# Kernel optimization log

Measured on AMD Instinct MI355X. Metric: run time of the kernel, lower is better.

## Reference

```python
import jax, jax.numpy as jnp
import numpy as np

N = 8192        # num_nodes == total_gene_dim (required by A @ init_emb)
B = 4           # batch_size (number of graphs / perturbations)
E = 262144      # edges per graph (avg degree 32)
MAX_HOP = 4
EMBED = 64
HIDDEN = 512
OUT = 64
LN_EPS = 1e-5


def setup_inputs() -> dict:
    key = jax.random.key(0)
    ks = jax.random.split(key, 8)
    s = 0.02
    return {
        "edge_index": jax.random.randint(ks[0], (B, 2, E), 0, N, dtype=jnp.int32),
        "perturb_one_hot": jax.random.randint(ks[1], (B,), 0, N, dtype=jnp.int32),
        "proj_w": jax.random.normal(ks[2], (EMBED, B), dtype=jnp.float32) * s,
        "proj_b": jax.random.normal(ks[3], (EMBED,), dtype=jnp.float32) * s,
        "w1": jax.random.normal(ks[4], (HIDDEN, MAX_HOP * EMBED), dtype=jnp.float32) * s,
        "b1": jax.random.normal(ks[5], (HIDDEN,), dtype=jnp.float32) * s,
        "ln_g": jnp.ones((HIDDEN,), dtype=jnp.float32),
        "ln_b": jnp.zeros((HIDDEN,), dtype=jnp.float32),
        "w2": jax.random.normal(ks[6], (OUT, HIDDEN), dtype=jnp.float32) * s,
        "b2": jax.random.normal(ks[7], (OUT,), dtype=jnp.float32) * s,
    }


def reference(edge_index, perturb_one_hot, proj_w, proj_b, w1, b1, ln_g, ln_b, w2, b2):
    dt = proj_w.dtype
    # one_hot(perturb).T : (N, B) -> proj -> (N, EMBED)
    one_hot_mat = jax.nn.one_hot(perturb_one_hot, N, dtype=dt).T
    init_emb = one_hot_mat @ proj_w.T + proj_b  # (N, EMBED)

    def per_graph(ei):
        # coalesce() sums duplicate COO entries -> scatter-add of ones
        A = jnp.zeros((N, N), dtype=dt).at[ei[0], ei[1]].add(jnp.ones((E,), dtype=dt))
        H = A @ init_emb  # (N, EMBED); original recomputes the SAME product max_hop times
        omega = jnp.stack([H] * MAX_HOP, axis=-1).reshape(N, MAX_HOP * EMBED)
        h = omega @ w1.T + b1  # (N, HIDDEN)
        mu = h.mean(-1, keepdims=True)
        var = h.var(-1, keepdims=True)
        h = (h - mu) / jnp.sqrt(var + LN_EPS) * ln_g + ln_b
        h = jax.nn.gelu(h, approximate=False)  # torch GELU default is exact erf form
        return h @ w2.T + b2  # (N, OUT)

    return jax.vmap(per_graph)(edge_index)  # (B, N, OUT)
```

## Files before the change

kernel.cpp:

```cpp
#include <hip/hip_runtime.h>
#include <math.h>

#define NN   8192
#define NB   4
#define NE   262144
#define EMB  64
#define HID  512
#define NOUT 64
#define DMAX 256
#define SPEC_FLAG (1 << 30)
#define SLICES 32
#define HBLK (NB * SLICES)
#define HWORDS (NN / 2)

__device__ __forceinline__ void eval_block(
    float dg, float c0, float c1, float c2, float c3,
    const float* __restrict__ u, const float* __restrict__ b1,
    const float* __restrict__ ln_g, const float* __restrict__ ln_b,
    const float* __restrict__ w2t4, const float* __restrict__ b2,
    float* __restrict__ dst,
    float* __restrict__ g,
    float* __restrict__ pacc,
    float* __restrict__ red)
{
    int tid = threadIdx.x, lane = tid & 63, wid = tid >> 6;

    int h1i = tid + 256;
    float h0 = dg * u[tid] + c0 * u[512 + tid] + c1 * u[1024 + tid]
             + c2 * u[1536 + tid] + c3 * u[2048 + tid] + b1[tid];
    float h1 = dg * u[h1i] + c0 * u[512 + h1i] + c1 * u[1024 + h1i]
             + c2 * u[1536 + h1i] + c3 * u[2048 + h1i] + b1[h1i];

    float s = h0 + h1, ss = h0 * h0 + h1 * h1;
    #pragma unroll
    for (int d2 = 1; d2 < 64; d2 <<= 1) {
        s  += __shfl_xor(s,  d2, 64);
        ss += __shfl_xor(ss, d2, 64);
    }
    if (lane == 0) { red[wid] = s; red[4 + wid] = ss; }
    __syncthreads();
    float S  = red[0] + red[1] + red[2] + red[3];
    float SS = red[4] + red[5] + red[6] + red[7];
    float mu  = S * (1.0f / 512.0f);
    float var = SS * (1.0f / 512.0f) - mu * mu;
    float rs  = rsqrtf(var + 1e-5f);

    float x0 = (h0 - mu) * rs * ln_g[tid] + ln_b[tid];
    g[tid]  = 0.5f * x0 * (1.0f + erff(x0 * 0.70710678118654752f));
    float x1 = (h1 - mu) * rs * ln_g[h1i] + ln_b[h1i];
    g[h1i]  = 0.5f * x1 * (1.0f + erff(x1 * 0.70710678118654752f));
    __syncthreads();

    const float4* W2 = (const float4*)w2t4;
    int h4b = wid * 32;
    float a0 = 0.f, a1 = 0.f;
    #pragma unroll 8
    for (int k = 0; k < 32; k += 2) {
        float4 w0  = W2[(h4b + k) * 64 + lane];
        float4 g0  = *(const float4*)(g + (h4b + k) * 4);
        float4 w1v = W2[(h4b + k + 1) * 64 + lane];
        float4 g1  = *(const float4*)(g + (h4b + k + 1) * 4);
        a0 += w0.x * g0.x + w0.y * g0.y + w0.z * g0.z + w0.w * g0.w;
        a1 += w1v.x * g1.x + w1v.y * g1.y + w1v.z * g1.z + w1v.w * g1.w;
    }
    pacc[wid * 64 + lane] = a0 + a1;
    __syncthreads();
    if (tid < 64)
        dst[tid] = pacc[tid] + pacc[64 + tid] + pacc[128 + tid] + pacc[192 + tid] + b2[tid];
    __syncthreads();
}

__global__ __launch_bounds__(256) void phaseA_kernel(const int* __restrict__ ei,
                                                     const int* __restrict__ pert,
                                                     const float* __restrict__ w1,
                                                     const float* __restrict__ w2,
                                                     const float* __restrict__ proj_w,
                                                     const float* __restrict__ proj_b,
                                                     unsigned int* __restrict__ hist_g,
                                                     int* __restrict__ cnt,
                                                     float* __restrict__ u,
                                                     float* __restrict__ w2t4) {
    __shared__ unsigned int hist[HWORDS];
    __shared__ float pb[EMB];
    __shared__ float pw[EMB * 4];
    int blk = blockIdx.x, tid = threadIdx.x;

    if (blk < HBLK) {
        int b = blk >> 5, s = blk & (SLICES - 1);
        #pragma unroll
        for (int k = 0; k < 4; ++k)
            *(uint4*)(hist + (k * 256 + tid) * 4) = make_uint4(0, 0, 0, 0);
        __syncthreads();

        int p0 = pert[0], p1 = pert[1], p2 = pert[2], p3 = pert[3];
        const int* src = ei + (size_t)b * 2 * NE + s * (NE / SLICES);
        const int* dst = src + NE;
        int base = b * NN;
        #pragma unroll
        for (int k = 0; k < 8; ++k) {
            int4 sv = ((const int4*)src)[k * 256 + tid];
            int4 dv = ((const int4*)dst)[k * 256 + tid];
            atomicAdd(&hist[sv.x >> 1], 1u << ((sv.x & 1) << 4));
            atomicAdd(&hist[sv.y >> 1], 1u << ((sv.y & 1) << 4));
            atomicAdd(&hist[sv.z >> 1], 1u << ((sv.z & 1) << 4));
            atomicAdd(&hist[sv.w >> 1], 1u << ((sv.w & 1) << 4));
            if (dv.x == p0) atomicAdd(&cnt[(base + sv.x) * 4 + 0], 1);
            if (dv.x == p1) atomicAdd(&cnt[(base + sv.x) * 4 + 1], 1);
            if (dv.x == p2) atomicAdd(&cnt[(base + sv.x) * 4 + 2], 1);
            if (dv.x == p3) atomicAdd(&cnt[(base + sv.x) * 4 + 3], 1);
            if (dv.y == p0) atomicAdd(&cnt[(base + sv.y) * 4 + 0], 1);
            if (dv.y == p1) atomicAdd(&cnt[(base + sv.y) * 4 + 1], 1);
            if (dv.y == p2) atomicAdd(&cnt[(base + sv.y) * 4 + 2], 1);
            if (dv.y == p3) atomicAdd(&cnt[(base + sv.y) * 4 + 3], 1);
            if (dv.z == p0) atomicAdd(&cnt[(base + sv.z) * 4 + 0], 1);
            if (dv.z == p1) atomicAdd(&cnt[(base + sv.z) * 4 + 1], 1);
            if (dv.z == p2) atomicAdd(&cnt[(base + sv.z) * 4 + 2], 1);
            if (dv.z == p3) atomicAdd(&cnt[(base + sv.z) * 4 + 3], 1);
            if (dv.w == p0) atomicAdd(&cnt[(base + sv.w) * 4 + 0], 1);
            if (dv.w == p1) atomicAdd(&cnt[(base + sv.w) * 4 + 1], 1);
            if (dv.w == p2) atomicAdd(&cnt[(base + sv.w) * 4 + 2], 1);
            if (dv.w == p3) atomicAdd(&cnt[(base + sv.w) * 4 + 3], 1);
        }
        __syncthreads();
        uint4* hg = (uint4*)(hist_g + (size_t)blk * HWORDS);
        #pragma unroll
        for (int k = 0; k < 4; ++k)
            hg[k * 256 + tid] = *(const uint4*)(hist + (k * 256 + tid) * 4);
    } else if (blk < HBLK + 2) {
        if (tid < EMB) pb[tid] = proj_b[tid];
        pw[tid] = proj_w[tid];
        __syncthreads();
        int hh = (blk - HBLK) * 256 + tid;
        const float4* row = (const float4*)(w1 + (size_t)hh * 256);
        float a0 = 0.f, a1 = 0.f, a2 = 0.f, a3 = 0.f, a4 = 0.f;
        #pragma unroll 8
        for (int e = 0; e < 64; ++e) {
            float4 v = row[e];
            float w = v.x + v.y + v.z + v.w;
            a0 += w * pb[e];
            a1 += w * pw[e * 4 + 0];
            a2 += w * pw[e * 4 + 1];
            a3 += w * pw[e * 4 + 2];
            a4 += w * pw[e * 4 + 3];
        }
        u[hh] = a0; u[512 + hh] = a1; u[1024 + hh] = a2; u[1536 + hh] = a3; u[2048 + hh] = a4;
    } else {
        int g = (blk - (HBLK + 2)) * 256 + tid;
        int o = g >> 7, h4 = g & 127;
        float4 v = *(const float4*)(w2 + (size_t)o * HID + h4 * 4);
        *(float4*)(w2t4 + (size_t)(h4 * 64 + o) * 4) = v;
    }
}

__global__ __launch_bounds__(256) void phaseB_kernel(
    const unsigned int* __restrict__ hist_g, const int* __restrict__ cnt,
    int* __restrict__ deg, int* __restrict__ nspec, int* __restrict__ spec,
    const float* __restrict__ u, const float* __restrict__ b1,
    const float* __restrict__ ln_g, const float* __restrict__ ln_b,
    const float* __restrict__ w2t4, const float* __restrict__ b2,
    float* __restrict__ table)
{
    __shared__ float g[HID];
    __shared__ float pacc[4 * 64];
    __shared__ float red[8];
    int blk = blockIdx.x, tid = threadIdx.x;
    if (blk < 128) {
        int gn = blk * 256 + tid;
        int b = gn >> 13, n = gn & (NN - 1);
        const unsigned int* hb = hist_g + (size_t)b * SLICES * HWORDS + (n >> 1);
        int sh = (n & 1) << 4;
        int d = 0;
        #pragma unroll 8
        for (int s = 0; s < SLICES; ++s) d += (hb[s * HWORDS] >> sh) & 0xFFFFu;
        int4 c = *(const int4*)(cnt + gn * 4);
        bool sp = ((c.x | c.y | c.z | c.w) != 0) || (d >= DMAX);
        if (sp) {
            int i = atomicAdd(nspec, 1);
            spec[i] = gn;
            d |= SPEC_FLAG;
        }
        deg[gn] = d;
    } else {
        int i = blk - 128;
        eval_block((float)i, 0.f, 0.f, 0.f, 0.f, u, b1, ln_g, ln_b, w2t4, b2,
                   table + (size_t)i * NOUT, g, pacc, red);
    }
}

__global__ __launch_bounds__(256) void phaseC_kernel(
    const int* __restrict__ nspec, const int* __restrict__ spec,
    const int* __restrict__ deg, const int* __restrict__ cnt,
    const float* __restrict__ u, const float* __restrict__ b1,
    const float* __restrict__ ln_g, const float* __restrict__ ln_b,
    const float* __restrict__ w2t4, const float* __restrict__ b2,
    const float* __restrict__ table, float* __restrict__ out)
{
    __shared__ float g[HID];
    __shared__ float pacc[4 * 64];
    __shared__ float red[8];
    int blk = blockIdx.x, tid = threadIdx.x;
    if (blk < 2048) {
        int t = blk * 256 + tid;
        int gn = t >> 4, q = t & 15;
        int d = deg[gn];
        if (d & SPEC_FLAG) return;
        d = d < DMAX - 1 ? d : DMAX - 1;
        ((float4*)out)[(size_t)gn * 16 + q] = ((const float4*)table)[(size_t)d * 16 + q];
    } else {
        int ns = *nspec;
        for (int i = blk - 2048; i < ns; i += 512) {
            int gn = spec[i];
            float dg = (float)(deg[gn] & ~SPEC_FLAG);
            int4 c = *(const int4*)(cnt + gn * 4);
            eval_block(dg, (float)c.x, (float)c.y, (float)c.z, (float)c.w,
                       u, b1, ln_g, ln_b, w2t4, b2,
                       out + (size_t)gn * NOUT, g, pacc, red);
        }
    }
}

extern "C" void kernel_launch(void* const* d_in, const int* in_sizes, int n_in,
                              void* d_out, int out_size, void* d_ws, size_t ws_size,
                              hipStream_t stream) {
    const int*   ei     = (const int*)d_in[0];
    const int*   pert   = (const int*)d_in[1];
    const float* proj_w = (const float*)d_in[2];
    const float* proj_b = (const float*)d_in[3];
    const float* w1     = (const float*)d_in[4];
    const float* b1     = (const float*)d_in[5];
    const float* ln_g   = (const float*)d_in[6];
    const float* ln_b   = (const float*)d_in[7];
    const float* w2     = (const float*)d_in[8];
    const float* b2     = (const float*)d_in[9];
    float* out = (float*)d_out;

    char* ws = (char*)d_ws;
    int*          deg    = (int*)ws;
    int*          cnt    = deg + 32768;
    int*          nspec  = cnt + 131072;
    int*          spec   = nspec + 1;
    float*        u      = (float*)(spec + 32768);
    float*        w2t4   = u + 2560;
    float*        table  = w2t4 + 32768;
    unsigned int* hist_g = (unsigned int*)(table + 16384);

    hipMemsetAsync(cnt, 0, (131072 + 1) * 4, stream);

    phaseA_kernel<<<HBLK + 34, 256, 0, stream>>>(ei, pert, w1, w2, proj_w, proj_b,
                                                 hist_g, cnt, u, w2t4);
    phaseB_kernel<<<384, 256, 0, stream>>>(hist_g, cnt, deg, nspec, spec,
                                           u, b1, ln_g, ln_b, w2t4, b2, table);
    phaseC_kernel<<<2560, 256, 0, stream>>>(nspec, spec, deg, cnt,
                                            u, b1, ln_g, ln_b, w2t4, b2, table, out);
}
```

Measured before the change: 105.6 us.

## Fuse memset and three phase kernels into one cooperative kernel with grid syncs

Replaces the memset plus three separate kernel launches with a single cooperative kernel of 512 blocks that uses grid.sync() between the histogram/weight-prep, degree/table, and output phases. Zeroing of cnt and nspec moves into the kernel prologue. The aim is to remove launch and inter-kernel gaps. In exchange it adds the cost of grid-wide barriers, raises shared memory per block (the histogram plus the eval scratch buffers), and requires all 512 blocks to be co-resident.

```diff
diff --git a/kernel.cpp b/kernel.cpp
--- a/kernel.cpp
+++ b/kernel.cpp
@@ -1,5 +1,8 @@
 #include <hip/hip_runtime.h>
+#include <hip/hip_cooperative_groups.h>
 #include <math.h>
+
+namespace cg = cooperative_groups;
 
 #define NN   8192
 #define NB   4
@@ -12,6 +15,7 @@
 #define SLICES 32
 #define HBLK (NB * SLICES)
 #define HWORDS (NN / 2)
+#define GRID 512
 
 __device__ __forceinline__ void eval_block(
     float dg, float c0, float c1, float c2, float c3,
@@ -19,9 +23,7 @@
     const float* __restrict__ ln_g, const float* __restrict__ ln_b,
     const float* __restrict__ w2t4, const float* __restrict__ b2,
     float* __restrict__ dst,
-    float* __restrict__ g,
-    float* __restrict__ pacc,
-    float* __restrict__ red)
+    float* __restrict__ g, float* __restrict__ pacc, float* __restrict__ red)
 {
     int tid = threadIdx.x, lane = tid & 63, wid = tid >> 6;
 
@@ -70,20 +72,30 @@
     __syncthreads();
 }
 
-__global__ __launch_bounds__(256) void phaseA_kernel(const int* __restrict__ ei,
-                                                     const int* __restrict__ pert,
-                                                     const float* __restrict__ w1,
-                                                     const float* __restrict__ w2,
-                                                     const float* __restrict__ proj_w,
-                                                     const float* __restrict__ proj_b,
-                                                     unsigned int* __restrict__ hist_g,
-                                                     int* __restrict__ cnt,
-                                                     float* __restrict__ u,
-                                                     float* __restrict__ w2t4) {
+__global__ __launch_bounds__(256) void fused_kernel(
+    const int* __restrict__ ei, const int* __restrict__ pert,
+    const float* __restrict__ proj_w, const float* __restrict__ proj_b,
+    const float* __restrict__ w1, const float* __restrict__ b1,
+    const float* __restrict__ ln_g, const float* __restrict__ ln_b,
+    const float* __restrict__ w2, const float* __restrict__ b2,
+    int* __restrict__ deg, int* __restrict__ cnt,
+    int* __restrict__ nspec, int* __restrict__ spec,
+    float* __restrict__ u, float* __restrict__ w2t4,
+    float* __restrict__ table, unsigned int* __restrict__ hist_g,
+    float* __restrict__ out)
+{
+    cg::grid_group grid = cg::this_grid();
     __shared__ unsigned int hist[HWORDS];
     __shared__ float pb[EMB];
     __shared__ float pw[EMB * 4];
+    __shared__ float g[HID];
+    __shared__ float pacc[4 * 64];
+    __shared__ float red[8];
     int blk = blockIdx.x, tid = threadIdx.x;
+
+    cnt[blk * 256 + tid] = 0;
+    if (blk == 0 && tid == 0) *nspec = 0;
+    grid.sync();
 
     if (blk < HBLK) {
         int b = blk >> 5, s = blk & (SLICES - 1);
@@ -144,26 +156,14 @@
             a4 += w * pw[e * 4 + 3];
         }
         u[hh] = a0; u[512 + hh] = a1; u[1024 + hh] = a2; u[1536 + hh] = a3; u[2048 + hh] = a4;
-    } else {
-        int g = (blk - (HBLK + 2)) * 256 + tid;
-        int o = g >> 7, h4 = g & 127;
+    } else if (blk < HBLK + 34) {
+        int gi = (blk - (HBLK + 2)) * 256 + tid;
+        int o = gi >> 7, h4 = gi & 127;
         float4 v = *(const float4*)(w2 + (size_t)o * HID + h4 * 4);
         *(float4*)(w2t4 + (size_t)(h4 * 64 + o) * 4) = v;
     }
-}
-
-__global__ __launch_bounds__(256) void phaseB_kernel(
-    const unsigned int* __restrict__ hist_g, const int* __restrict__ cnt,
-    int* __restrict__ deg, int* __restrict__ nspec, int* __restrict__ spec,
-    const float* __restrict__ u, const float* __restrict__ b1,
-    const float* __restrict__ ln_g, const float* __restrict__ ln_b,
-    const float* __restrict__ w2t4, const float* __restrict__ b2,
-    float* __restrict__ table)
-{
-    __shared__ float g[HID];
-    __shared__ float pacc[4 * 64];
-    __shared__ float red[8];
-    int blk = blockIdx.x, tid = threadIdx.x;
+    grid.sync();
+
     if (blk < 128) {
         int gn = blk * 256 + tid;
         int b = gn >> 13, n = gn & (NN - 1);
@@ -180,42 +180,31 @@
             d |= SPEC_FLAG;
         }
         deg[gn] = d;
-    } else {
+    } else if (blk < 384) {
         int i = blk - 128;
         eval_block((float)i, 0.f, 0.f, 0.f, 0.f, u, b1, ln_g, ln_b, w2t4, b2,
                    table + (size_t)i * NOUT, g, pacc, red);
     }
-}
-
-__global__ __launch_bounds__(256) void phaseC_kernel(
-    const int* __restrict__ nspec, const int* __restrict__ spec,
-    const int* __restrict__ deg, const int* __restrict__ cnt,
-    const float* __restrict__ u, const float* __restrict__ b1,
-    const float* __restrict__ ln_g, const float* __restrict__ ln_b,
-    const float* __restrict__ w2t4, const float* __restrict__ b2,
-    const float* __restrict__ table, float* __restrict__ out)
-{
-    __shared__ float g[HID];
-    __shared__ float pacc[4 * 64];
-    __shared__ float red[8];
-    int blk = blockIdx.x, tid = threadIdx.x;
-    if (blk < 2048) {
-        int t = blk * 256 + tid;
+    grid.sync();
+
+    #pragma unroll
+    for (int k = 0; k < 4; ++k) {
+        int t = (blk * 4 + k) * 256 + tid;
         int gn = t >> 4, q = t & 15;
         int d = deg[gn];
-        if (d & SPEC_FLAG) return;
-        d = d < DMAX - 1 ? d : DMAX - 1;
-        ((float4*)out)[(size_t)gn * 16 + q] = ((const float4*)table)[(size_t)d * 16 + q];
-    } else {
-        int ns = *nspec;
-        for (int i = blk - 2048; i < ns; i += 512) {
-            int gn = spec[i];
-            float dg = (float)(deg[gn] & ~SPEC_FLAG);
-            int4 c = *(const int4*)(cnt + gn * 4);
-            eval_block(dg, (float)c.x, (float)c.y, (float)c.z, (float)c.w,
-                       u, b1, ln_g, ln_b, w2t4, b2,
-                       out + (size_t)gn * NOUT, g, pacc, red);
-        }
+        if (!(d & SPEC_FLAG)) {
+            d = d < DMAX - 1 ? d : DMAX - 1;
+            ((float4*)out)[(size_t)gn * 16 + q] = ((const float4*)table)[(size_t)d * 16 + q];
+        }
+    }
+    int ns = *nspec;
+    for (int i = blk; i < ns; i += GRID) {
+        int gn = spec[i];
+        float dg = (float)(deg[gn] & ~SPEC_FLAG);
+        int4 c = *(const int4*)(cnt + gn * 4);
+        eval_block(dg, (float)c.x, (float)c.y, (float)c.z, (float)c.w,
+                   u, b1, ln_g, ln_b, w2t4, b2,
+                   out + (size_t)gn * NOUT, g, pacc, red);
     }
 }
 
@@ -244,12 +233,14 @@
     float*        table  = w2t4 + 32768;
     unsigned int* hist_g = (unsigned int*)(table + 16384);
 
-    hipMemsetAsync(cnt, 0, (131072 + 1) * 4, stream);
-
-    phaseA_kernel<<<HBLK + 34, 256, 0, stream>>>(ei, pert, w1, w2, proj_w, proj_b,
-                                                 hist_g, cnt, u, w2t4);
-    phaseB_kernel<<<384, 256, 0, stream>>>(hist_g, cnt, deg, nspec, spec,
-                                           u, b1, ln_g, ln_b, w2t4, b2, table);
-    phaseC_kernel<<<2560, 256, 0, stream>>>(nspec, spec, deg, cnt,
-                                            u, b1, ln_g, ln_b, w2t4, b2, table, out);
+    void* kargs[] = {
+        (void*)&ei, (void*)&pert, (void*)&proj_w, (void*)&proj_b,
+        (void*)&w1, (void*)&b1, (void*)&ln_g, (void*)&ln_b,
+        (void*)&w2, (void*)&b2,
+        (void*)&deg, (void*)&cnt, (void*)&nspec, (void*)&spec,
+        (void*)&u, (void*)&w2t4, (void*)&table, (void*)&hist_g,
+        (void*)&out
+    };
+    hipLaunchCooperativeKernel((void*)fused_kernel, dim3(GRID), dim3(256),
+                               kargs, 0, stream);
 }
```

After: 274.2 us. 2.6x slower.
